# Performance work log

Measured on AMD Instinct MI355X. Metric: run time of the kernel, lower is better.

The kernel has to match this reference:

```python
import jax, jax.numpy as jnp
import numpy as np

N_NODES = 50000
N_EDGES = 800000
D_IN, D_HID, D_OUT = 128, 512, 128


def setup_inputs() -> dict:
    key = jax.random.key(0)
    k1, k2, k3, k4, k5 = jax.random.split(key, 5)
    nh = jax.random.normal(k1, (N_NODES, D_IN), dtype=jnp.float32)
    eh = jax.random.normal(k2, (N_EDGES, D_IN), dtype=jnp.float32)
    edge_index = jax.random.randint(k3, (2, N_EDGES), 0, N_NODES, dtype=jnp.int64)
    # 2-layer GIN MLP params (Linear(128->512), relu, Linear(512->128)), bias=True
    W1 = jax.random.normal(k4, (D_IN, D_HID), dtype=jnp.float32) * (1.0 / np.sqrt(D_IN))
    b1 = jnp.zeros((D_HID,), dtype=jnp.float32)
    W2 = jax.random.normal(k5, (D_HID, D_OUT), dtype=jnp.float32) * (1.0 / np.sqrt(D_HID))
    b2 = jnp.zeros((D_OUT,), dtype=jnp.float32)
    eps = jnp.zeros((1,), dtype=jnp.float32)  # nf_eps parameter, init 0.0
    return {"nh": nh, "eh": eh, "W1": W1, "b1": b1, "W2": W2, "b2": b2,
            "eps": eps, "edge_index": edge_index}


def reference(nh, eh, W1, b1, W2, b2, eps, edge_index):
    src, dst = edge_index[0], edge_index[1]
    # gather src features, scatter-add into dst nodes: [N, D_IN]
    nz = jax.ops.segment_sum(nh[src], dst, num_segments=nh.shape[0])
    n_h = (1.0 + eps) * nh + nz  # epsilon-scaled residual
    # GIN MLP: Linear -> relu -> Linear (dropout=0, eval)
    h = jax.nn.relu(jnp.einsum("nd,dh->nh", n_h, W1) + b1)
    n_h = jnp.einsum("nh,ho->no", h, W2) + b2
    return (n_h, eh)
```

## Files before the change

### kernel.cpp

```cpp
#include <hip/hip_runtime.h>

#define N_NODES 50000
#define N_EDGES 800000
#define D_IN 128
#define D_HID 512
#define D_OUT 128

#define EH_FLOAT4 (N_EDGES * (D_IN / 4))
#define CPB 4096

#define C_PREP 400
#define C_HIST 750
#define C_SCAN 200
#define C_FILL 750
#define C_GATH 2600
#define C_GEMMF 1550

typedef __attribute__((ext_vector_type(8))) short short8v;
typedef __attribute__((ext_vector_type(4))) float f32x4;

__device__ __forceinline__ unsigned short f2bf(float f) {
    union { float f; unsigned u; } v; v.f = f;
    unsigned u = v.u;
    return (unsigned short)((u + 0x7FFFu + ((u >> 16) & 1u)) >> 16);
}
__device__ __forceinline__ float bf2f(unsigned u16) {
    union { unsigned u; float f; } v; v.u = u16 << 16;
    return v.f;
}

__device__ __forceinline__ long long interleave(long long b, long long C,
                                                long long T, long long* w) {
    long long cb = (C == 0) ? 0 : (b * C) / T;
    bool isCopy = C != 0 && ((b + 1) * C) / T > cb;
    *w = b - cb;
    return isCopy ? cb : -1;
}

__device__ __forceinline__ void copy_chunk(const float4* __restrict__ src,
                                           float4* __restrict__ dst,
                                           long long base, long long cb) {
    const f32x4* s = (const f32x4*)src;
    f32x4* d = (f32x4*)dst;
    long long o = base + cb * CPB + threadIdx.x;
#pragma unroll
    for (int i = 0; i < 16; ++i) {
        f32x4 v = __builtin_nontemporal_load(&s[o + i * 256]);
        __builtin_nontemporal_store(v, &d[o + i * 256]);
    }
}

__global__ __launch_bounds__(256) void k_prep(const float4* __restrict__ nh,
                                              const float* __restrict__ W1,
                                              const float* __restrict__ W2,
                                              uint2* __restrict__ nh16,
                                              unsigned short* __restrict__ W1T,
                                              unsigned short* __restrict__ W2T,
                                              int* __restrict__ counts,
                                              int* __restrict__ pub,
                                              const float4* __restrict__ csrc,
                                              float4* __restrict__ cdst,
                                              long long copyBase, int copyC) {
    long long w;
    const int W = 6250 + 256 + 256 + 196;
    long long cb = interleave(blockIdx.x, copyC, W + copyC, &w);
    if (cb >= 0) { copy_chunk(csrc, cdst, copyBase, cb); return; }
    int tid = threadIdx.x;
    if (w < 6250) {
        int i = (int)w * 256 + tid;
        if (i < N_NODES * (D_IN / 4)) {
            float4 a = nh[i];
            uint2 r;
            r.x = (unsigned)f2bf(a.x) | ((unsigned)f2bf(a.y) << 16);
            r.y = (unsigned)f2bf(a.z) | ((unsigned)f2bf(a.w) << 16);
            nh16[i] = r;
        }
    } else if (w < 6506) {
        int i = (int)(w - 6250) * 256 + tid;
        int n = i >> 7, k = i & 127;
        W1T[i] = f2bf(W1[k * D_HID + n]);
    } else if (w < 6762) {
        int i = (int)(w - 6506) * 256 + tid;
        int n = i >> 9, k = i & 511;
        W2T[i] = f2bf(W2[k * D_OUT + n]);
    } else {
        int i = (int)(w - 6762) * 256 + tid;
        if (i <= N_NODES) counts[i] = 0;
        if (i < 196) pub[i] = 0;
    }
}


__global__ __launch_bounds__(256) void k_hist(const int* __restrict__ ei,
                                              int* __restrict__ counts,
                                              const float4* __restrict__ csrc,
                                              float4* __restrict__ cdst,
                                              long long copyBase, int copyC) {
    long long w;
    const int W = (N_EDGES + 255) / 256;
    long long cb = interleave(blockIdx.x, copyC, W + copyC, &w);
    if (cb >= 0) { copy_chunk(csrc, cdst, copyBase, cb); return; }
    int e = (int)w * 256 + threadIdx.x;
    if (e >= N_EDGES) return;
    atomicAdd(&counts[ei[N_EDGES + e]], 1);
}

__global__ __launch_bounds__(256) void k_scan_lb(const int* __restrict__ counts,
                                                 int* __restrict__ offs,
                                                 int* __restrict__ cursors,
                                                 int* __restrict__ pub,
                                                 const float4* __restrict__ csrc,
                                                 float4* __restrict__ cdst,
                                                 long long copyBase, int copyC) {
    long long w;
    long long cb = interleave(blockIdx.x, copyC, 196 + copyC, &w);
    if (cb >= 0) { copy_chunk(csrc, cdst, copyBase, cb); return; }
    int b = (int)w;
    __shared__ int s[256];
    __shared__ int r[256];
    int tid = threadIdx.x;
    int i = b * 256 + tid;
    int v = (i < N_NODES) ? counts[i] : 0;
    s[tid] = v;
    __syncthreads();
#pragma unroll
    for (int off = 1; off < 256; off <<= 1) {
        int t = (tid >= off) ? s[tid - off] : 0;
        __syncthreads();
        if (tid >= off) s[tid] += t;
        __syncthreads();
    }
    if (tid == 255)
        __hip_atomic_store(&pub[b], s[255] + 1, __ATOMIC_RELEASE,
                           __HIP_MEMORY_SCOPE_AGENT);
    int contrib = 0;
    if (tid < b) {
        int p;
        do {
            p = __hip_atomic_load(&pub[tid], __ATOMIC_ACQUIRE,
                                  __HIP_MEMORY_SCOPE_AGENT);
        } while (p == 0);
        contrib = p - 1;
    }
    r[tid] = contrib;
    __syncthreads();
#pragma unroll
    for (int off = 128; off > 0; off >>= 1) {
        if (tid < off) r[tid] += r[tid + off];
        __syncthreads();
    }
    int prefix = r[0];
    if (i < N_NODES) {
        int o = (s[tid] - v) + prefix;
        offs[i] = o;
        cursors[i] = o;
    }
    if (b == 0 && tid == 0) offs[N_NODES] = N_EDGES;
}

__global__ __launch_bounds__(256) void k_fill(const int* __restrict__ ei,
                                              int* __restrict__ cursors,
                                              int* __restrict__ csr_src,
                                              const float4* __restrict__ csrc,
                                              float4* __restrict__ cdst,
                                              long long copyBase, int copyC) {
    long long w;
    const int W = (N_EDGES + 255) / 256;
    long long cb = interleave(blockIdx.x, copyC, W + copyC, &w);
    if (cb >= 0) { copy_chunk(csrc, cdst, copyBase, cb); return; }
    int e = (int)w * 256 + threadIdx.x;
    if (e >= N_EDGES) return;
    int dst = ei[N_EDGES + e];
    int pos = atomicAdd(&cursors[dst], 1);
    csr_src[pos] = ei[e];
}

__global__ __launch_bounds__(256) void k_gather16(const unsigned* __restrict__ nh16,
                                                  const int* __restrict__ csr_src,
                                                  const int* __restrict__ offs,
                                                  const float* __restrict__ eps,
                                                  unsigned* __restrict__ acc16,
                                                  const float4* __restrict__ csrc,
                                                  float4* __restrict__ cdst,
                                                  long long copyBase, int copyC) {
    long long w;
    const int W = (N_NODES + 3) / 4;
    long long cb = interleave(blockIdx.x, copyC, W + copyC, &w);
    if (cb >= 0) { copy_chunk(csrc, cdst, copyBase, cb); return; }
    int node = (int)w * 4 + (threadIdx.x >> 6);
    if (node >= N_NODES) return;
    int lane = threadIdx.x & 63;
    int beg = offs[node], end = offs[node + 1];
    float sx = 0.f, sy = 0.f;
    int j = beg;
    for (; j + 3 < end; j += 4) {
        int s0 = csr_src[j];
        int s1 = csr_src[j + 1];
        int s2 = csr_src[j + 2];
        int s3 = csr_src[j + 3];
        unsigned v0 = nh16[(size_t)s0 * 64 + lane];
        unsigned v1 = nh16[(size_t)s1 * 64 + lane];
        unsigned v2 = nh16[(size_t)s2 * 64 + lane];
        unsigned v3 = nh16[(size_t)s3 * 64 + lane];
        sx += bf2f(v0 & 0xFFFFu) + bf2f(v1 & 0xFFFFu) +
              bf2f(v2 & 0xFFFFu) + bf2f(v3 & 0xFFFFu);
        sy += bf2f(v0 >> 16) + bf2f(v1 >> 16) + bf2f(v2 >> 16) + bf2f(v3 >> 16);
    }
    for (; j < end; ++j) {
        unsigned v0 = nh16[(size_t)csr_src[j] * 64 + lane];
        sx += bf2f(v0 & 0xFFFFu);
        sy += bf2f(v0 >> 16);
    }
    float sc = 1.0f + eps[0];
    unsigned m = nh16[(size_t)node * 64 + lane];
    sx += sc * bf2f(m & 0xFFFFu);
    sy += sc * bf2f(m >> 16);
    acc16[(size_t)node * 64 + lane] =
        (unsigned)f2bf(sx) | ((unsigned)f2bf(sy) << 16);
}

__global__ __launch_bounds__(256) void k_copy_eh(const float4* __restrict__ src,
                                                 float4* __restrict__ dst) {
    int i = blockIdx.x * 256 + threadIdx.x;
    if (i >= EH_FLOAT4) return;
    const f32x4* s = (const f32x4*)src;
    f32x4* d = (f32x4*)dst;
    f32x4 v = __builtin_nontemporal_load(&s[i]);
    __builtin_nontemporal_store(v, &d[i]);
}

__global__ __launch_bounds__(256, 2) void gemm_fused(
        const unsigned short* __restrict__ A,
        const unsigned short* __restrict__ W1t,
        const float* __restrict__ b1,
        const unsigned short* __restrict__ W2t,
        const float* __restrict__ b2,
        float* __restrict__ Cout,
        int M,
        const float4* __restrict__ csrc, float4* __restrict__ cdst,
        long long copyBase, int copyC, int workW) {
    long long w;
    long long cb = interleave(blockIdx.x, copyC, workW + copyC, &w);
    if (cb >= 0) { copy_chunk(csrc, cdst, copyBase, cb); return; }

    __shared__ unsigned short Hs[128][136];

    const int tid = threadIdx.x;
    const int m0 = (int)w * 128;
    const int wid = tid >> 6;
    const int lane = tid & 63;
    const int wr = wid >> 1;
    const int wc = wid & 1;
    const int l15 = lane & 15;
    const int kg = lane >> 4;

    short8v af[4][4];
#pragma unroll
    for (int i = 0; i < 4; ++i) {
        int gr = m0 + wr * 64 + i * 16 + l15;
        const unsigned short* Ar = A + (size_t)gr * D_IN + kg * 8;
        if (gr < M) {
#pragma unroll
            for (int ks = 0; ks < 4; ++ks)
                af[ks][i] = *(const short8v*)(Ar + ks * 32);
        } else {
#pragma unroll
            for (int ks = 0; ks < 4; ++ks)
                af[ks][i] = (short8v){0, 0, 0, 0, 0, 0, 0, 0};
        }
    }

    f32x4 acc2[4][4];
#pragma unroll
    for (int i = 0; i < 4; ++i)
#pragma unroll
        for (int j = 0; j < 4; ++j) acc2[i][j] = (f32x4){0.f, 0.f, 0.f, 0.f};

    for (int ht = 0; ht < 4; ++ht) {
        __syncthreads();

#pragma unroll
        for (int j = 0; j < 4; ++j) {
            const int lc = wc * 64 + j * 16 + l15;
            const unsigned short* Wr = W1t + (size_t)(ht * 128 + lc) * D_IN + kg * 8;
            f32x4 a1[4];
#pragma unroll
            for (int i = 0; i < 4; ++i) a1[i] = (f32x4){0.f, 0.f, 0.f, 0.f};
#pragma unroll
            for (int ks = 0; ks < 4; ++ks) {
                short8v bbj = *(const short8v*)(Wr + ks * 32);
#pragma unroll
                for (int i = 0; i < 4; ++i)
                    a1[i] = __builtin_amdgcn_mfma_f32_16x16x32_bf16(
                        af[ks][i], bbj, a1[i], 0, 0, 0);
            }
            float bv = b1[ht * 128 + lc];
#pragma unroll
            for (int i = 0; i < 4; ++i)
#pragma unroll
                for (int q = 0; q < 4; ++q) {
                    float v = a1[i][q] + bv;
                    Hs[wr * 64 + i * 16 + kg * 4 + q][lc] = f2bf(fmaxf(v, 0.f));
                }
        }
        __syncthreads();

#pragma unroll
        for (int ks = 0; ks < 4; ++ks) {
            short8v ha[4], bb[4];
#pragma unroll
            for (int i = 0; i < 4; ++i)
                ha[i] = *(const short8v*)&Hs[wr * 64 + i * 16 + l15][ks * 32 + kg * 8];
#pragma unroll
            for (int j = 0; j < 4; ++j)
                bb[j] = *(const short8v*)(W2t + (size_t)(wc * 64 + j * 16 + l15) * D_HID
                                          + ht * 128 + ks * 32 + kg * 8);
#pragma unroll
            for (int i = 0; i < 4; ++i)
#pragma unroll
                for (int j = 0; j < 4; ++j)
                    acc2[i][j] = __builtin_amdgcn_mfma_f32_16x16x32_bf16(
                        ha[i], bb[j], acc2[i][j], 0, 0, 0);
        }
    }

#pragma unroll
    for (int j = 0; j < 4; ++j) {
        int gc = wc * 64 + j * 16 + l15;
        float bv = b2[gc];
#pragma unroll
        for (int i = 0; i < 4; ++i) {
#pragma unroll
            for (int q = 0; q < 4; ++q) {
                int gr = m0 + wr * 64 + i * 16 + kg * 4 + q;
                if (gr >= M) continue;
                Cout[(size_t)gr * D_OUT + gc] = acc2[i][j][q] + bv;
            }
        }
    }
}

extern "C" void kernel_launch(void* const* d_in, const int* in_sizes, int n_in,
                              void* d_out, int out_size, void* d_ws, size_t ws_size,
                              hipStream_t stream) {
    const float* nh  = (const float*)d_in[0];
    const float* eh  = (const float*)d_in[1];
    const float* W1  = (const float*)d_in[2];
    const float* b1  = (const float*)d_in[3];
    const float* W2  = (const float*)d_in[4];
    const float* b2  = (const float*)d_in[5];
    const float* eps = (const float*)d_in[6];
    const int*   ei  = (const int*)d_in[7];

    float* out0 = (float*)d_out;
    float* out1 = out0 + (size_t)N_NODES * D_OUT;

    const size_t NEED = 36u << 20;
    bool useWs = (d_ws != nullptr) && (ws_size >= NEED);
    char* base = useWs ? (char*)d_ws : (char*)out1;

    unsigned*       nh16  = (unsigned*)(base);
    unsigned*       acc16 = (unsigned*)(base + (13u << 20));
    unsigned short* w1t   = (unsigned short*)(base + (26u << 20));
    unsigned short* w2t   = (unsigned short*)(base + (27u << 20));
    int*            ibase = (int*)(base + (28u << 20));
    int* offs    = ibase;
    int* cursors = ibase + 65536;
    int* pub     = ibase + 131072;
    int* csr_src = ibase + 262144;

    const float4* csrc = (const float4*)eh;
    float4*       cdst = (float4*)out1;

    int c0 = useWs ? C_PREP  : 0;  long long b0 = 0;
    int c1 = useWs ? C_HIST  : 0;  long long b1c = (long long)(C_PREP) * CPB;
    int c2 = useWs ? C_SCAN  : 0;  long long b2c = (long long)(C_PREP + C_HIST) * CPB;
    int c3 = useWs ? C_FILL  : 0;  long long b3c = (long long)(C_PREP + C_HIST + C_SCAN) * CPB;
    int c4 = useWs ? C_GATH  : 0;  long long b4c = (long long)(C_PREP + C_HIST + C_SCAN + C_FILL) * CPB;
    int c5 = useWs ? C_GEMMF : 0;  long long b5c = (long long)(C_PREP + C_HIST + C_SCAN + C_FILL + C_GATH) * CPB;

    k_prep<<<6958 + c0, 256, 0, stream>>>((const float4*)nh, W1, W2,
        (uint2*)nh16, w1t, w2t, cursors, pub, csrc, cdst, b0, c0);

    k_hist<<<3125 + c1, 256, 0, stream>>>(ei, cursors, csrc, cdst, b1c, c1);
    k_scan_lb<<<196 + c2, 256, 0, stream>>>(cursors, offs, cursors, pub,
                                            csrc, cdst, b2c, c2);
    k_fill<<<3125 + c3, 256, 0, stream>>>(ei, cursors, csr_src, csrc, cdst, b3c, c3);
    k_gather16<<<12500 + c4, 256, 0, stream>>>(nh16, csr_src, offs, eps, acc16,
                                               csrc, cdst, b4c, c4);

    const int WFblocks = (N_NODES + 127) / 128;
    gemm_fused<<<WFblocks + c5, 256, 0, stream>>>(
        (const unsigned short*)acc16, w1t, b1, w2t, b2, out0,
        N_NODES, csrc, cdst, b5c, c5, WFblocks);

    if (!useWs) {
        k_copy_eh<<<(EH_FLOAT4 + 255) / 256, 256, 0, stream>>>(csrc, cdst);
    }
}
```

Measured before the change: 301.5 us.

## Replace interleaved eh copy chunks with a standalone upfront copy kernel

The eh passthrough copy was previously split into chunks interleaved inside every pipeline kernel's grid so it could overlap with the compute stages. This change drops that interleaving and launches one dedicated chunked copy kernel before the pipeline. It removes the interleave bookkeeping and block-mix imbalance, but the roughly 400 MB copy no longer overlaps with the compute kernels and is serialized ahead of them.

```diff
diff --git a/kernel.cpp b/kernel.cpp
--- a/kernel.cpp
+++ b/kernel.cpp
@@ -8,13 +8,7 @@
 
 #define EH_FLOAT4 (N_EDGES * (D_IN / 4))
 #define CPB 4096
-
-#define C_PREP 400
-#define C_HIST 750
-#define C_SCAN 200
-#define C_FILL 750
-#define C_GATH 2600
-#define C_GEMMF 1550
+#define NCHUNKS 6250
 
 typedef __attribute__((ext_vector_type(8))) short short8v;
 typedef __attribute__((ext_vector_type(4))) float f32x4;
@@ -48,6 +42,11 @@
         f32x4 v = __builtin_nontemporal_load(&s[o + i * 256]);
         __builtin_nontemporal_store(v, &d[o + i * 256]);
     }
+}
+
+__global__ __launch_bounds__(256) void k_copy_all(const float4* __restrict__ src,
+                                                  float4* __restrict__ dst) {
+    copy_chunk(src, dst, 0, blockIdx.x);
 }
 
 __global__ __launch_bounds__(256) void k_prep(const float4* __restrict__ nh,
@@ -219,16 +218,6 @@
         (unsigned)f2bf(sx) | ((unsigned)f2bf(sy) << 16);
 }
 
-__global__ __launch_bounds__(256) void k_copy_eh(const float4* __restrict__ src,
-                                                 float4* __restrict__ dst) {
-    int i = blockIdx.x * 256 + threadIdx.x;
-    if (i >= EH_FLOAT4) return;
-    const f32x4* s = (const f32x4*)src;
-    f32x4* d = (f32x4*)dst;
-    f32x4 v = __builtin_nontemporal_load(&s[i]);
-    __builtin_nontemporal_store(v, &d[i]);
-}
-
 __global__ __launch_bounds__(256, 2) void gemm_fused(
         const unsigned short* __restrict__ A,
         const unsigned short* __restrict__ W1t,
@@ -372,29 +361,26 @@
     const float4* csrc = (const float4*)eh;
     float4*       cdst = (float4*)out1;
 
-    int c0 = useWs ? C_PREP  : 0;  long long b0 = 0;
-    int c1 = useWs ? C_HIST  : 0;  long long b1c = (long long)(C_PREP) * CPB;
-    int c2 = useWs ? C_SCAN  : 0;  long long b2c = (long long)(C_PREP + C_HIST) * CPB;
-    int c3 = useWs ? C_FILL  : 0;  long long b3c = (long long)(C_PREP + C_HIST + C_SCAN) * CPB;
-    int c4 = useWs ? C_GATH  : 0;  long long b4c = (long long)(C_PREP + C_HIST + C_SCAN + C_FILL) * CPB;
-    int c5 = useWs ? C_GEMMF : 0;  long long b5c = (long long)(C_PREP + C_HIST + C_SCAN + C_FILL + C_GATH) * CPB;
-
-    k_prep<<<6958 + c0, 256, 0, stream>>>((const float4*)nh, W1, W2,
-        (uint2*)nh16, w1t, w2t, cursors, pub, csrc, cdst, b0, c0);
-
-    k_hist<<<3125 + c1, 256, 0, stream>>>(ei, cursors, csrc, cdst, b1c, c1);
-    k_scan_lb<<<196 + c2, 256, 0, stream>>>(cursors, offs, cursors, pub,
-                                            csrc, cdst, b2c, c2);
-    k_fill<<<3125 + c3, 256, 0, stream>>>(ei, cursors, csr_src, csrc, cdst, b3c, c3);
-    k_gather16<<<12500 + c4, 256, 0, stream>>>(nh16, csr_src, offs, eps, acc16,
-                                               csrc, cdst, b4c, c4);
+    if (useWs) {
+        k_copy_all<<<NCHUNKS, 256, 0, stream>>>(csrc, cdst);
+    }
+
+    k_prep<<<6958, 256, 0, stream>>>((const float4*)nh, W1, W2,
+        (uint2*)nh16, w1t, w2t, cursors, pub, csrc, cdst, 0, 0);
+
+    k_hist<<<3125, 256, 0, stream>>>(ei, cursors, csrc, cdst, 0, 0);
+    k_scan_lb<<<196, 256, 0, stream>>>(cursors, offs, cursors, pub,
+                                       csrc, cdst, 0, 0);
+    k_fill<<<3125, 256, 0, stream>>>(ei, cursors, csr_src, csrc, cdst, 0, 0);
+    k_gather16<<<12500, 256, 0, stream>>>(nh16, csr_src, offs, eps, acc16,
+                                          csrc, cdst, 0, 0);
 
     const int WFblocks = (N_NODES + 127) / 128;
-    gemm_fused<<<WFblocks + c5, 256, 0, stream>>>(
+    gemm_fused<<<WFblocks, 256, 0, stream>>>(
         (const unsigned short*)acc16, w1t, b1, w2t, b2, out0,
-        N_NODES, csrc, cdst, b5c, c5, WFblocks);
+        N_NODES, csrc, cdst, 0, 0, WFblocks);
 
     if (!useWs) {
-        k_copy_eh<<<(EH_FLOAT4 + 255) / 256, 256, 0, stream>>>(csrc, cdst);
-    }
-}
+        k_copy_all<<<NCHUNKS, 256, 0, stream>>>(csrc, cdst);
+    }
+}
```

Result: slower. 337.7 us (+12.0%).

## Bucket CSR edges by source-node range to improve gather locality

Applied to the files above, without the earlier changes.

The CSR build now keys each edge by (src/6250, dst), giving eight source-range passes per destination node. The gather kernel walks each node's neighbours pass by pass, so at a given moment concurrent waves tend to touch sources from the same 1/8 of the node table. The intent is better L2 hit rates on the random feature gather. In exchange the counts and scan arrays grow eightfold (400k entries, about 1563 scan blocks with a longer serial publish chain), and the gather inner loop gets more offset loads and shorter unrolls.

```diff
diff --git a/kernel.cpp b/kernel.cpp
--- a/kernel.cpp
+++ b/kernel.cpp
@@ -5,6 +5,10 @@
 #define D_IN 128
 #define D_HID 512
 #define D_OUT 128
+
+#define NPASS 8
+#define NCOUNT (NPASS * N_NODES)
+#define SCAN_BLOCKS ((NCOUNT + 255) / 256)
 
 #define EH_FLOAT4 (N_EDGES * (D_IN / 4))
 #define CPB 4096
@@ -62,7 +66,7 @@
                                               float4* __restrict__ cdst,
                                               long long copyBase, int copyC) {
     long long w;
-    const int W = 6250 + 256 + 256 + 196;
+    const int W = 6250 + 256 + 256 + SCAN_BLOCKS;
     long long cb = interleave(blockIdx.x, copyC, W + copyC, &w);
     if (cb >= 0) { copy_chunk(csrc, cdst, copyBase, cb); return; }
     int tid = threadIdx.x;
@@ -85,8 +89,8 @@
         W2T[i] = f2bf(W2[k * D_OUT + n]);
     } else {
         int i = (int)(w - 6762) * 256 + tid;
-        if (i <= N_NODES) counts[i] = 0;
-        if (i < 196) pub[i] = 0;
+        if (i < NCOUNT) counts[i] = 0;
+        if (i < SCAN_BLOCKS) pub[i] = 0;
     }
 }
 
@@ -102,7 +106,9 @@
     if (cb >= 0) { copy_chunk(csrc, cdst, copyBase, cb); return; }
     int e = (int)w * 256 + threadIdx.x;
     if (e >= N_EDGES) return;
-    atomicAdd(&counts[ei[N_EDGES + e]], 1);
+    int src = ei[e];
+    int dst = ei[N_EDGES + e];
+    atomicAdd(&counts[(src / 6250) * N_NODES + dst], 1);
 }
 
 __global__ __launch_bounds__(256) void k_scan_lb(const int* __restrict__ counts,
@@ -113,14 +119,14 @@
                                                  float4* __restrict__ cdst,
                                                  long long copyBase, int copyC) {
     long long w;
-    long long cb = interleave(blockIdx.x, copyC, 196 + copyC, &w);
+    long long cb = interleave(blockIdx.x, copyC, SCAN_BLOCKS + copyC, &w);
     if (cb >= 0) { copy_chunk(csrc, cdst, copyBase, cb); return; }
     int b = (int)w;
     __shared__ int s[256];
     __shared__ int r[256];
     int tid = threadIdx.x;
     int i = b * 256 + tid;
-    int v = (i < N_NODES) ? counts[i] : 0;
+    int v = (i < NCOUNT) ? counts[i] : 0;
     s[tid] = v;
     __syncthreads();
 #pragma unroll
@@ -134,13 +140,13 @@
         __hip_atomic_store(&pub[b], s[255] + 1, __ATOMIC_RELEASE,
                            __HIP_MEMORY_SCOPE_AGENT);
     int contrib = 0;
-    if (tid < b) {
+    for (int pb = tid; pb < b; pb += 256) {
         int p;
         do {
-            p = __hip_atomic_load(&pub[tid], __ATOMIC_ACQUIRE,
+            p = __hip_atomic_load(&pub[pb], __ATOMIC_ACQUIRE,
                                   __HIP_MEMORY_SCOPE_AGENT);
         } while (p == 0);
-        contrib = p - 1;
+        contrib += p - 1;
     }
     r[tid] = contrib;
     __syncthreads();
@@ -150,12 +156,12 @@
         __syncthreads();
     }
     int prefix = r[0];
-    if (i < N_NODES) {
+    if (i < NCOUNT) {
         int o = (s[tid] - v) + prefix;
         offs[i] = o;
         cursors[i] = o;
     }
-    if (b == 0 && tid == 0) offs[N_NODES] = N_EDGES;
+    if (b == 0 && tid == 0) offs[NCOUNT] = N_EDGES;
 }
 
 __global__ __launch_bounds__(256) void k_fill(const int* __restrict__ ei,
@@ -170,9 +176,10 @@
     if (cb >= 0) { copy_chunk(csrc, cdst, copyBase, cb); return; }
     int e = (int)w * 256 + threadIdx.x;
     if (e >= N_EDGES) return;
+    int src = ei[e];
     int dst = ei[N_EDGES + e];
-    int pos = atomicAdd(&cursors[dst], 1);
-    csr_src[pos] = ei[e];
+    int pos = atomicAdd(&cursors[(src / 6250) * N_NODES + dst], 1);
+    csr_src[pos] = src;
 }
 
 __global__ __launch_bounds__(256) void k_gather16(const unsigned* __restrict__ nh16,
@@ -190,26 +197,25 @@
     int node = (int)w * 4 + (threadIdx.x >> 6);
     if (node >= N_NODES) return;
     int lane = threadIdx.x & 63;
-    int beg = offs[node], end = offs[node + 1];
     float sx = 0.f, sy = 0.f;
-    int j = beg;
-    for (; j + 3 < end; j += 4) {
-        int s0 = csr_src[j];
-        int s1 = csr_src[j + 1];
-        int s2 = csr_src[j + 2];
-        int s3 = csr_src[j + 3];
-        unsigned v0 = nh16[(size_t)s0 * 64 + lane];
-        unsigned v1 = nh16[(size_t)s1 * 64 + lane];
-        unsigned v2 = nh16[(size_t)s2 * 64 + lane];
-        unsigned v3 = nh16[(size_t)s3 * 64 + lane];
-        sx += bf2f(v0 & 0xFFFFu) + bf2f(v1 & 0xFFFFu) +
-              bf2f(v2 & 0xFFFFu) + bf2f(v3 & 0xFFFFu);
-        sy += bf2f(v0 >> 16) + bf2f(v1 >> 16) + bf2f(v2 >> 16) + bf2f(v3 >> 16);
-    }
-    for (; j < end; ++j) {
-        unsigned v0 = nh16[(size_t)csr_src[j] * 64 + lane];
-        sx += bf2f(v0 & 0xFFFFu);
-        sy += bf2f(v0 >> 16);
+#pragma unroll 1
+    for (int p = 0; p < NPASS; ++p) {
+        int idx = p * N_NODES + node;
+        int beg = offs[idx], end = offs[idx + 1];
+        int j = beg;
+        for (; j + 1 < end; j += 2) {
+            int s0 = csr_src[j];
+            int s1 = csr_src[j + 1];
+            unsigned v0 = nh16[(size_t)s0 * 64 + lane];
+            unsigned v1 = nh16[(size_t)s1 * 64 + lane];
+            sx += bf2f(v0 & 0xFFFFu) + bf2f(v1 & 0xFFFFu);
+            sy += bf2f(v0 >> 16) + bf2f(v1 >> 16);
+        }
+        if (j < end) {
+            unsigned v0 = nh16[(size_t)csr_src[j] * 64 + lane];
+            sx += bf2f(v0 & 0xFFFFu);
+            sy += bf2f(v0 >> 16);
+        }
     }
     float sc = 1.0f + eps[0];
     unsigned m = nh16[(size_t)node * 64 + lane];
@@ -365,9 +371,9 @@
     unsigned short* w2t   = (unsigned short*)(base + (27u << 20));
     int*            ibase = (int*)(base + (28u << 20));
     int* offs    = ibase;
-    int* cursors = ibase + 65536;
-    int* pub     = ibase + 131072;
-    int* csr_src = ibase + 262144;
+    int* cursors = ibase + 524288;
+    int* pub     = ibase + 1048576;
+    int* csr_src = ibase + 1064960;
 
     const float4* csrc = (const float4*)eh;
     float4*       cdst = (float4*)out1;
@@ -379,12 +385,12 @@
     int c4 = useWs ? C_GATH  : 0;  long long b4c = (long long)(C_PREP + C_HIST + C_SCAN + C_FILL) * CPB;
     int c5 = useWs ? C_GEMMF : 0;  long long b5c = (long long)(C_PREP + C_HIST + C_SCAN + C_FILL + C_GATH) * CPB;
 
-    k_prep<<<6958 + c0, 256, 0, stream>>>((const float4*)nh, W1, W2,
+    k_prep<<<8325 + c0, 256, 0, stream>>>((const float4*)nh, W1, W2,
         (uint2*)nh16, w1t, w2t, cursors, pub, csrc, cdst, b0, c0);
 
     k_hist<<<3125 + c1, 256, 0, stream>>>(ei, cursors, csrc, cdst, b1c, c1);
-    k_scan_lb<<<196 + c2, 256, 0, stream>>>(cursors, offs, cursors, pub,
-                                            csrc, cdst, b2c, c2);
+    k_scan_lb<<<SCAN_BLOCKS + c2, 256, 0, stream>>>(cursors, offs, cursors, pub,
+                                                    csrc, cdst, b2c, c2);
     k_fill<<<3125 + c3, 256, 0, stream>>>(ei, cursors, csr_src, csrc, cdst, b3c, c3);
     k_gather16<<<12500 + c4, 256, 0, stream>>>(nh16, csr_src, offs, eps, acc16,
                                                csrc, cdst, b4c, c4);
```

Result: slower. 511.3 us (+69.6%).
